# Performance work log

Measured on AMD Instinct MI355X. Metric: run time of the kernel, lower is better.

The kernel has to match this reference:

```python
import jax, jax.numpy as jnp
import numpy as np

N, E, B, BLOCK = 100000, 1600000, 8, 12500
IN, HID, K, OUT = 128, 128, 4, 2
EPS = 1e-15


def setup_inputs() -> dict:
    key = jax.random.key(0)
    ks = jax.random.split(key, 14)
    x = jax.random.normal(ks[0], (N, IN), jnp.float32)
    # edges constrained within each graph's contiguous node block
    src = jax.random.randint(ks[1], (E,), 0, N)
    off = jax.random.randint(ks[2], (E,), 0, BLOCK)
    dst = (src // BLOCK) * BLOCK + off
    edge_index = jnp.stack([src, dst])
    batch = jnp.arange(N) // BLOCK
    s = 0.02
    params = dict(
        W_root1=jax.random.normal(ks[3], (IN, HID), jnp.float32) * s,
        W_rel1=jax.random.normal(ks[4], (IN, HID), jnp.float32) * s,
        b_rel1=jnp.zeros((HID,), jnp.float32),
        W_pool=jax.random.normal(ks[5], (HID, K), jnp.float32) * s,
        b_pool=jnp.zeros((K,), jnp.float32),
        W_rel3=jax.random.normal(ks[6], (HID, HID), jnp.float32) * s,
        b_rel3=jnp.zeros((HID,), jnp.float32),
        W_root3=jax.random.normal(ks[7], (HID, HID), jnp.float32) * s,
        W_lin1=jax.random.normal(ks[8], (HID, HID), jnp.float32) * s,
        b_lin1=jnp.zeros((HID,), jnp.float32),
        W_lin2=jax.random.normal(ks[9], (HID, OUT), jnp.float32) * s,
        b_lin2=jnp.zeros((OUT,), jnp.float32),
    )
    return dict(x=x, edge_index=edge_index, batch=batch, **params)


def _forward(x, edge_index, batch, W_root1, W_rel1, b_rel1, W_pool, b_pool,
             W_rel3, b_rel3, W_root3, W_lin1, b_lin1, W_lin2, b_lin2):
    src, dst = edge_index[0], edge_index[1]
    # GraphConv (aggr='add'): lin_rel(sum_j x_j) + lin_root(x)
    agg = jax.ops.segment_sum(x[src], dst, num_segments=N)  # [N, IN]
    h = jax.nn.relu(agg @ W_rel1 + b_rel1 + x @ W_root1)    # [N, HID]
    # cluster assignment
    s = jax.nn.softmax(h @ W_pool + b_pool, axis=-1)        # [N, K]
    # pooled node features: out[b] = S_b^T X_b  -> [B, K, HID]
    out = jax.ops.segment_sum(s[:, :, None] * h[:, None, :], batch, num_segments=B)
    # coarsened adjacency: out_adj[b] = S_b^T A_b S_b (A[dst, src] = 1 per edge)
    e_graph = batch[dst]
    contrib = s[dst][:, :, None] * s[src][:, None, :]       # [E, K, K]
    out_adj = jax.ops.segment_sum(contrib, e_graph, num_segments=B)  # [B, K, K]
    # mincut loss
    mincut_num = jnp.einsum('bkk->b', out_adj)
    deg = jax.ops.segment_sum(jnp.ones((E,), x.dtype), dst, num_segments=N)
    mincut_den = jax.ops.segment_sum(deg * jnp.sum(s * s, axis=-1), batch, num_segments=B)
    mc_loss = jnp.mean(-(mincut_num / mincut_den))
    # orthogonality loss
    ss = jax.ops.segment_sum(s[:, :, None] * s[:, None, :], batch, num_segments=B)  # [B,K,K]
    ss_norm = jnp.linalg.norm(ss, axis=(1, 2), keepdims=True)
    i_s = jnp.eye(K, dtype=x.dtype)
    o_loss = jnp.mean(jnp.linalg.norm(ss / ss_norm - i_s / jnp.sqrt(jnp.float32(K)), axis=(1, 2)))
    # fix and normalize coarsened adjacency
    out_adj = out_adj * (1.0 - i_s)  # zero diagonal
    d = jnp.sqrt(jnp.sum(out_adj, axis=-1)) + EPS  # [B, K]
    out_adj = out_adj / d[:, None, :] / d[:, :, None]
    # DenseGraphConv (aggr='add'): lin_rel(adj @ x) + lin_root(x)
    x2 = jnp.einsum('bkl,blc->bkc', out_adj, out) @ W_rel3 + b_rel3 + out @ W_root3
    x2 = jnp.mean(x2, axis=1)  # [B, HID]
    x2 = jax.nn.relu(x2 @ W_lin1 + b_lin1)
    logits = x2 @ W_lin2 + b_lin2
    return jax.nn.log_softmax(logits, axis=-1), mc_loss, o_loss, s, out_adj


def reference(x, edge_index, batch, W_root1, W_rel1, b_rel1, W_pool, b_pool,
              W_rel3, b_rel3, W_root3, W_lin1, b_lin1, W_lin2, b_lin2):
    return _forward(x, edge_index, batch, W_root1, W_rel1, b_rel1, W_pool, b_pool,
                    W_rel3, b_rel3, W_root3, W_lin1, b_lin1, W_lin2, b_lin2)
```

## Files before the change

kernel.cpp:

```cpp
#include <hip/hip_runtime.h>

#define NN     100000
#define EE     1600000
#define NB     8
#define BLK    12500
#define HID    128
#define KC     4
#define CHUNKS 196
#define NTILE  49
#define NBIN   392
#define GCAPS  5120

typedef __attribute__((ext_vector_type(8))) short bf16x8;
typedef __attribute__((ext_vector_type(4))) float f32x4;

__device__ __forceinline__ ushort f2bf(float f) {
  uint u = __float_as_uint(f);
  return (ushort)((u + 0x7FFFu + ((u >> 16) & 1u)) >> 16);
}
__device__ __forceinline__ float bf2f(ushort h) {
  return __uint_as_float(((uint)h) << 16);
}

#define GLL16(g, l) \
  __builtin_amdgcn_global_load_lds((const __attribute__((address_space(1))) void*)(g), \
                                   (__attribute__((address_space(3))) void*)(l), 16, 0, 0)

__global__ __launch_bounds__(256) void k_prep_x(const float4* __restrict__ x4,
                                                ushort* __restrict__ xb) {
  int i = blockIdx.x * 256 + threadIdx.x;
  float4 v = x4[i];
  ushort4 r;
  r.x = f2bf(v.x); r.y = f2bf(v.y); r.z = f2bf(v.z); r.w = f2bf(v.w);
  *(ushort4*)(xb + (size_t)i * 4) = r;
}

__global__ __launch_bounds__(256) void k_prep_w(const float* __restrict__ Wrel1,
                                                const float* __restrict__ Wroot1,
                                                ushort* __restrict__ Wt) {
  int col = blockIdx.x, k = threadIdx.x;
  float v = (k < 128) ? Wrel1[k * 128 + col] : Wroot1[(k - 128) * 128 + col];
  Wt[col * 256 + k] = f2bf(v);
}

__global__ __launch_bounds__(256) void k_bucket2(const int* __restrict__ ei,
                                                 int* __restrict__ sbcnt,
                                                 uint* __restrict__ gbuf) {
  __shared__ uint stage[8192];
  __shared__ int cnt[NBIN], start[NBIN + 1], rbase[NBIN];
  __shared__ int gtot[8], gb[8];
  const int t = threadIdx.x;
  for (int b = t; b < NBIN; b += 256) cnt[b] = 0;
  __syncthreads();
  const int e0 = blockIdx.x * 8192;
  uint pk[32]; int br[32];
#pragma unroll
  for (int i = 0; i < 32; ++i) {
    int e = e0 + i * 256 + t;
    bool val = (e < EE);
    int src = 0, dst = 0;
    if (val) {
      src = __builtin_nontemporal_load(ei + e);
      dst = __builtin_nontemporal_load(ei + EE + e);
    }
    int g = dst / BLK;
    int dl = dst - g * BLK;
    int sl = src - g * BLK;
    int bin = g * NTILE + (dl >> 8);
    pk[i] = ((uint)sl << 16) | (uint)dl;
    br[i] = val ? ((bin << 14) | atomicAdd(&cnt[bin], 1)) : -1;
  }
  __syncthreads();
  if (t < 8) {
    int s = 0;
    for (int k = 0; k < NTILE; ++k) s += cnt[t * NTILE + k];
    gtot[t] = s;
  }
  __syncthreads();
  if (t == 0) {
    int s = 0;
    for (int g = 0; g < 8; ++g) { gb[g] = s; s += gtot[g]; }
    start[NBIN] = s;
  }
  __syncthreads();
  if (t < 8) {
    int run = gb[t];
    for (int k = 0; k < NTILE; ++k) { start[t * NTILE + k] = run; run += cnt[t * NTILE + k]; }
  }
  __syncthreads();
  for (int b = t; b < NBIN; b += 256) rbase[b] = atomicAdd(&sbcnt[b], cnt[b]);
#pragma unroll
  for (int i = 0; i < 32; ++i) {
    if (br[i] >= 0) {
      int bin = br[i] >> 14, rank = br[i] & 16383;
      stage[start[bin] + rank] = pk[i];
    }
  }
  __syncthreads();
  const int total = start[NBIN];
  for (int j = t; j < total; j += 256) {
    int lo = 0, hi = NBIN - 1;
    while (lo < hi) { int mid = (lo + hi + 1) >> 1; if (j >= start[mid]) lo = mid; else hi = mid - 1; }
    gbuf[(size_t)lo * GCAPS + rbase[lo] + (j - start[lo])] = stage[j];
  }
}

__global__ __launch_bounds__(512) void k_scan392(const int* __restrict__ sbcnt,
                                                 int* __restrict__ sbbase) {
  __shared__ int sd[512];
  const int t = threadIdx.x;
  int v = (t < NBIN) ? sbcnt[t] : 0;
  sd[t] = v;
  __syncthreads();
  for (int s = 1; s < 512; s <<= 1) {
    int x = (t >= s) ? sd[t - s] : 0;
    __syncthreads();
    sd[t] += x;
    __syncthreads();
  }
  if (t < NBIN) sbbase[t] = sd[t] - v;
}

__global__ __launch_bounds__(256) void k_csr_tile(const uint* __restrict__ gbuf,
                                                  const int* __restrict__ sbcnt,
                                                  const int* __restrict__ sbbase,
                                                  int* __restrict__ rowptr,
                                                  int* __restrict__ count,
                                                  int* __restrict__ csr) {
  const int g = blockIdx.x & 7;
  const int tile = blockIdx.x >> 3;
  const int bin = g * NTILE + tile;
  const int m = sbcnt[bin];
  const int base = sbbase[bin];
  const int n0t = tile * 256;
  const int nt = min(256, BLK - n0t);
  __shared__ uint ent[GCAPS];
  __shared__ ushort srt[GCAPS];
  __shared__ int cnt[256], scn[256], cur[256];
  const int t = threadIdx.x;
  cnt[t] = 0;
  __syncthreads();
  const uint* buf = gbuf + (size_t)bin * GCAPS;
  for (int i = t; i < m; i += 256) {
    uint pk = buf[i];
    ent[i] = pk;
    atomicAdd(&cnt[(int)(pk & 0xFFFFu) - n0t], 1);
  }
  __syncthreads();
  int v = cnt[t];
  scn[t] = v;
  __syncthreads();
  for (int s = 1; s < 256; s <<= 1) {
    int x = (t >= s) ? scn[t - s] : 0;
    __syncthreads();
    scn[t] += x;
    __syncthreads();
  }
  int excl = scn[t] - v;
  cur[t] = excl;
  if (t < nt) {
    rowptr[g * BLK + n0t + t] = base + excl;
    count[g * BLK + n0t + t] = v;
  }
  __syncthreads();
  for (int i = t; i < m; i += 256) {
    uint pk = ent[i];
    int p = atomicAdd(&cur[(int)(pk & 0xFFFFu) - n0t], 1);
    srt[p] = (ushort)(pk >> 16);
  }
  __syncthreads();
  const int nb = g * BLK;
  for (int i = t; i < m; i += 256)
    csr[base + i] = nb + (int)srt[i];
}

__global__ __launch_bounds__(256) void k_agg2(const ushort* __restrict__ xb,
                                              const int* __restrict__ count,
                                              const int* __restrict__ rowptr,
                                              const int* __restrict__ csr,
                                              ushort* __restrict__ aggb) {
  const int xg = blockIdx.x & 7;
  const int j = blockIdx.x >> 3;
  const int half = threadIdx.x >> 5;
  const int lane = threadIdx.x & 31;
  const int ln = j * 8 + half;
  if (ln >= BLK) return;
  const int node = xg * BLK + ln;
  const int deg = count[node];
  const int* sl = csr + rowptr[node];
  int idx0 = (lane < deg) ? sl[lane] : 0;
  int idx1 = (32 + lane < deg) ? sl[32 + lane] : 0;

#define GETIDX(e) ((e) < 32 ? __shfl(idx0, (e), 32) \
                            : ((e) < 64 ? __shfl(idx1, (e) - 32, 32) : sl[(e)]))

  float A0 = 0.f, A1 = 0.f, A2 = 0.f, A3 = 0.f;
  float B0 = 0.f, B1 = 0.f, B2 = 0.f, B3 = 0.f;
  float C0 = 0.f, C1 = 0.f, C2 = 0.f, C3 = 0.f;
  float D0 = 0.f, D1 = 0.f, D2 = 0.f, D3 = 0.f;
  int e = 0;
  for (; e + 4 <= deg; e += 4) {
    int s0 = GETIDX(e + 0);
    int s1 = GETIDX(e + 1);
    int s2 = GETIDX(e + 2);
    int s3 = GETIDX(e + 3);
    ushort4 v0 = *(const ushort4*)(xb + (size_t)s0 * HID + lane * 4);
    ushort4 v1 = *(const ushort4*)(xb + (size_t)s1 * HID + lane * 4);
    ushort4 v2 = *(const ushort4*)(xb + (size_t)s2 * HID + lane * 4);
    ushort4 v3 = *(const ushort4*)(xb + (size_t)s3 * HID + lane * 4);
    A0 += bf2f(v0.x); A1 += bf2f(v0.y); A2 += bf2f(v0.z); A3 += bf2f(v0.w);
    B0 += bf2f(v1.x); B1 += bf2f(v1.y); B2 += bf2f(v1.z); B3 += bf2f(v1.w);
    C0 += bf2f(v2.x); C1 += bf2f(v2.y); C2 += bf2f(v2.z); C3 += bf2f(v2.w);
    D0 += bf2f(v3.x); D1 += bf2f(v3.y); D2 += bf2f(v3.z); D3 += bf2f(v3.w);
  }
  for (; e < deg; ++e) {
    int s0 = GETIDX(e);
    ushort4 v0 = *(const ushort4*)(xb + (size_t)s0 * HID + lane * 4);
    A0 += bf2f(v0.x); A1 += bf2f(v0.y); A2 += bf2f(v0.z); A3 += bf2f(v0.w);
  }
#undef GETIDX

  ushort* dstp = aggb + (size_t)node * HID + lane * 4;
  ushort4 r;
  r.x = f2bf(A0 + B0 + C0 + D0);
  r.y = f2bf(A1 + B1 + C1 + D1);
  r.z = f2bf(A2 + B2 + C2 + D2);
  r.w = f2bf(A3 + B3 + C3 + D3);
  *(ushort4*)dstp = r;
}

__global__ __launch_bounds__(256) void k_fused(
    const ushort* __restrict__ aggb, const ushort* __restrict__ xb,
    const ushort* __restrict__ Wt, const float* __restrict__ brel1,
    const float* __restrict__ Wpool, const float* __restrict__ bpool,
    const int* __restrict__ count, float* __restrict__ s_out,
    float* __restrict__ out_pool, float* __restrict__ ss_g,
    float* __restrict__ den_g) {
  __shared__ ushort Aag_s[64][128];
  __shared__ ushort Ax_s[64][128];
  __shared__ ushort hLb[64][136];
  __shared__ float outL[KC][HID];
  __shared__ float ssL[16];
  __shared__ float denL;

  const int t = threadIdx.x;
  const int bi = blockIdx.x;
  const int bG = bi & 7;
  const int chunk = bi >> 3;
  const int node0 = bG * BLK + chunk * 64;
  int nrows = BLK - chunk * 64;
  if (nrows > 64) nrows = 64;

  const int w = t >> 6;
  const int l = t & 63;

  {
    const int sub = l >> 4;
    const int c16 = l & 15;
#pragma unroll
    for (int i = 0; i < 4; ++i) {
      const int j = w * 4 + i;
      const int row = j * 4 + sub;
      const int rs = (row < nrows) ? row : (nrows - 1);
      const int boff = (c16 * 16) ^ ((row & 7) << 4);
      const ushort* ga = aggb + (size_t)(node0 + rs) * HID + (boff >> 1);
      const ushort* gx = xb + (size_t)(node0 + rs) * HID + (boff >> 1);
      GLL16(ga, &Aag_s[j * 4][0]);
      GLL16(gx, &Ax_s[j * 4][0]);
    }
  }

  for (int i = t; i < KC * HID; i += 256) ((float*)outL)[i] = 0.f;
  if (t < 16) ssL[t] = 0.f;
  if (t == 0) denL = 0.f;

  const int m16 = l & 15;
  const int gq = l >> 4;

  bf16x8 Breg[8][2];
#pragma unroll
  for (int kt = 0; kt < 8; ++kt)
#pragma unroll
    for (int fc = 0; fc < 2; ++fc)
      Breg[kt][fc] =
          *(const bf16x8*)(Wt + (size_t)(32 * w + 16 * fc + m16) * 256 + kt * 32 + 8 * gq);

  f32x4 acc[4][2];
#pragma unroll
  for (int fr = 0; fr < 4; ++fr)
#pragma unroll
    for (int fc = 0; fc < 2; ++fc) acc[fr][fc] = (f32x4){0.f, 0.f, 0.f, 0.f};

  asm volatile("s_waitcnt vmcnt(0)" ::: "memory");
  __syncthreads();

#pragma unroll
  for (int kt = 0; kt < 8; ++kt) {
    const int k4 = kt & 3;
    bf16x8 af[4];
#pragma unroll
    for (int fr = 0; fr < 4; ++fr) {
      const int r = 16 * fr + m16;
      const int ci = (k4 * 32 + gq * 8) ^ ((r & 7) << 3);
      af[fr] = (kt < 4) ? *(const bf16x8*)&Aag_s[r][ci]
                        : *(const bf16x8*)&Ax_s[r][ci];
    }
#pragma unroll
    for (int fr = 0; fr < 4; ++fr)
#pragma unroll
      for (int fc = 0; fc < 2; ++fc)
        acc[fr][fc] = __builtin_amdgcn_mfma_f32_16x16x32_bf16(af[fr], Breg[kt][fc],
                                                              acc[fr][fc], 0, 0, 0);
  }

  const float bc0 = brel1[32 * w + m16];
  const float bc1 = brel1[32 * w + 16 + m16];
#pragma unroll
  for (int fr = 0; fr < 4; ++fr)
#pragma unroll
    for (int fc = 0; fc < 2; ++fc)
#pragma unroll
      for (int r = 0; r < 4; ++r)
        hLb[16 * fr + 4 * gq + r][32 * w + 16 * fc + m16] =
            f2bf(fmaxf(acc[fr][fc][r] + (fc ? bc1 : bc0), 0.f));
  __syncthreads();

  const int g4 = t >> 4;
  const int c0 = (t & 15) << 2;
  const int li = t & 15;

  float h[4][8];
#pragma unroll
  for (int r = 0; r < 4; ++r) {
    ushort4 v0 = *(const ushort4*)&hLb[g4 * 4 + r][c0];
    ushort4 v1 = *(const ushort4*)&hLb[g4 * 4 + r][c0 + 64];
    h[r][0] = bf2f(v0.x); h[r][1] = bf2f(v0.y); h[r][2] = bf2f(v0.z); h[r][3] = bf2f(v0.w);
    h[r][4] = bf2f(v1.x); h[r][5] = bf2f(v1.y); h[r][6] = bf2f(v1.z); h[r][7] = bf2f(v1.w);
  }

  float wp[8][4];
#pragma unroll
  for (int j = 0; j < 8; ++j) {
    int col = c0 + (j & 3) + (j >> 2) * 64;
    float4 v = *(const float4*)(Wpool + col * 4);
    wp[j][0] = v.x; wp[j][1] = v.y; wp[j][2] = v.z; wp[j][3] = v.w;
  }
  float pp[4][4];
#pragma unroll
  for (int r = 0; r < 4; ++r)
#pragma unroll
    for (int k = 0; k < 4; ++k) pp[r][k] = 0.f;
#pragma unroll
  for (int r = 0; r < 4; ++r)
#pragma unroll
    for (int j = 0; j < 8; ++j)
#pragma unroll
      for (int k = 0; k < 4; ++k) pp[r][k] = fmaf(h[r][j], wp[j][k], pp[r][k]);
#pragma unroll
  for (int m = 1; m <= 8; m <<= 1)
#pragma unroll
    for (int r = 0; r < 4; ++r)
#pragma unroll
      for (int k = 0; k < 4; ++k) pp[r][k] += __shfl_xor(pp[r][k], m);

  float4 bp4 = *(const float4*)bpool;
  float bp[4] = {bp4.x, bp4.y, bp4.z, bp4.w};
  float sv[4][4];
#pragma unroll
  for (int r = 0; r < 4; ++r) {
    float p[4];
#pragma unroll
    for (int k = 0; k < 4; ++k) p[k] = pp[r][k] + bp[k];
    float mx = fmaxf(fmaxf(p[0], p[1]), fmaxf(p[2], p[3]));
    float e0 = expf(p[0] - mx), e1 = expf(p[1] - mx), e2 = expf(p[2] - mx), e3 = expf(p[3] - mx);
    float inv = 1.f / (e0 + e1 + e2 + e3);
    float valid = (g4 * 4 + r < nrows) ? 1.f : 0.f;
    sv[r][0] = e0 * inv * valid; sv[r][1] = e1 * inv * valid;
    sv[r][2] = e2 * inv * valid; sv[r][3] = e3 * inv * valid;
  }

  {
    int rW = li >> 2, kW = li & 3;
    if (g4 * 4 + rW < nrows) {
      int node = node0 + g4 * 4 + rW;
      float val = 0.f;
#pragma unroll
      for (int rr = 0; rr < 4; ++rr)
#pragma unroll
        for (int kk = 0; kk < 4; ++kk)
          if (li == rr * 4 + kk) val = sv[rr][kk];
      s_out[node * 4 + kW] = val;
    }
  }

  {
    int k1 = li >> 2, k2 = li & 3;
    float a1[4], a2[4];
#pragma unroll
    for (int rr = 0; rr < 4; ++rr) {
      float v1 = 0.f, v2 = 0.f;
#pragma unroll
      for (int kk = 0; kk < 4; ++kk) {
        if (k1 == kk) v1 = sv[rr][kk];
        if (k2 == kk) v2 = sv[rr][kk];
      }
      a1[rr] = v1; a2[rr] = v2;
    }
    float ssv = a1[0] * a2[0] + a1[1] * a2[1] + a1[2] * a2[2] + a1[3] * a2[3];
    atomicAdd(&ssL[li], ssv);
  }

  if (li == 0) {
    float dent = 0.f;
#pragma unroll
    for (int rr = 0; rr < 4; ++rr) {
      int rowg = g4 * 4 + rr;
      if (rowg < nrows) {
        float dg = (float)count[node0 + rowg];
        dent += dg * (sv[rr][0] * sv[rr][0] + sv[rr][1] * sv[rr][1] +
                      sv[rr][2] * sv[rr][2] + sv[rr][3] * sv[rr][3]);
      }
    }
    atomicAdd(&denL, dent);
  }

  float po[4][8];
#pragma unroll
  for (int k = 0; k < 4; ++k)
#pragma unroll
    for (int c = 0; c < 8; ++c) po[k][c] = 0.f;
#pragma unroll
  for (int k = 0; k < 4; ++k)
#pragma unroll
    for (int rr = 0; rr < 4; ++rr)
#pragma unroll
      for (int c = 0; c < 8; ++c) po[k][c] = fmaf(sv[rr][k], h[rr][c], po[k][c]);
#pragma unroll
  for (int k = 0; k < 4; ++k)
#pragma unroll
    for (int c = 0; c < 8; ++c) {
      po[k][c] += __shfl_xor(po[k][c], 16);
      po[k][c] += __shfl_xor(po[k][c], 32);
    }
  if ((t & 63) < 16) {
#pragma unroll
    for (int k = 0; k < 4; ++k)
#pragma unroll
      for (int c = 0; c < 8; ++c)
        atomicAdd(&outL[k][c0 + (c & 3) + (c >> 2) * 64], po[k][c]);
  }

  __syncthreads();
  for (int i = t; i < KC * HID; i += 256)
    atomicAdd(&out_pool[bG * KC * HID + i], ((const float*)outL)[i]);
  if (t < 16) atomicAdd(&ss_g[bG * 16 + t], ssL[t]);
  if (t == 0) atomicAdd(&den_g[bG], denL);
}

__global__ __launch_bounds__(256) void k_adj2(const int* __restrict__ count,
                                              const int* __restrict__ rowptr,
                                              const int* __restrict__ csr,
                                              const float* __restrict__ s,
                                              float* __restrict__ adjraw) {
  __shared__ float accL[4][2][16];
  const int t = threadIdx.x;
  if (t < 128) ((float*)accL)[t] = 0.f;
  __syncthreads();
  const int node = blockIdx.x * 256 + t;
  const int g0 = (blockIdx.x * 256) / BLK;
  if (node < NN) {
    const int gi = node / BLK - g0;
    const int deg = count[node];
    const int* sl = csr + rowptr[node];
    float A0 = 0.f, A1 = 0.f, A2 = 0.f, A3 = 0.f;
    float B0 = 0.f, B1 = 0.f, B2 = 0.f, B3 = 0.f;
    float C0 = 0.f, C1 = 0.f, C2 = 0.f, C3 = 0.f;
    float D0 = 0.f, D1 = 0.f, D2 = 0.f, D3 = 0.f;
    int e = 0;
    for (; e + 4 <= deg; e += 4) {
      int s0 = sl[e + 0], s1 = sl[e + 1], s2 = sl[e + 2], s3 = sl[e + 3];
      float4 v0 = *(const float4*)(s + (size_t)s0 * 4);
      float4 v1 = *(const float4*)(s + (size_t)s1 * 4);
      float4 v2 = *(const float4*)(s + (size_t)s2 * 4);
      float4 v3 = *(const float4*)(s + (size_t)s3 * 4);
      A0 += v0.x; A1 += v0.y; A2 += v0.z; A3 += v0.w;
      B0 += v1.x; B1 += v1.y; B2 += v1.z; B3 += v1.w;
      C0 += v2.x; C1 += v2.y; C2 += v2.z; C3 += v2.w;
      D0 += v3.x; D1 += v3.y; D2 += v3.z; D3 += v3.w;
    }
    for (; e < deg; ++e) {
      float4 v0 = *(const float4*)(s + (size_t)sl[e] * 4);
      A0 += v0.x; A1 += v0.y; A2 += v0.z; A3 += v0.w;
    }
    float t0 = A0 + B0 + C0 + D0;
    float t1 = A1 + B1 + C1 + D1;
    float t2 = A2 + B2 + C2 + D2;
    float t3 = A3 + B3 + C3 + D3;
    float4 sn = *(const float4*)(s + (size_t)node * 4);
    float* base = accL[t >> 6][gi];
#pragma unroll
    for (int i = 0; i < 16; ++i) {
      int idx = (i + t) & 15;
      int hi = idx >> 2, lo = idx & 3;
      float a = (hi == 0) ? sn.x : (hi == 1) ? sn.y : (hi == 2) ? sn.z : sn.w;
      float b = (lo == 0) ? t0 : (lo == 1) ? t1 : (lo == 2) ? t2 : t3;
      atomicAdd(base + idx, a * b);
    }
  }
  __syncthreads();
  if (t < 32) {
    int gi = t >> 4, i = t & 15, gg = g0 + gi;
    if (gg < NB) {
      float v = accL[0][gi][i] + accL[1][gi][i] + accL[2][gi][i] + accL[3][gi][i];
      atomicAdd(&adjraw[gg * 16 + i], v);
    }
  }
}

__global__ __launch_bounds__(128) void k_graph(
    const float* __restrict__ out_pool, const float* __restrict__ adjraw,
    const float* __restrict__ den_g, const float* __restrict__ ss_g,
    const float* __restrict__ Wrel3, const float* __restrict__ brel3,
    const float* __restrict__ Wroot3, const float* __restrict__ Wlin1,
    const float* __restrict__ blin1, const float* __restrict__ Wlin2,
    const float* __restrict__ blin2, float* __restrict__ d_out,
    float* __restrict__ scratch) {
  const int b = blockIdx.x, t = threadIdx.x;
  __shared__ float adjL[16], adjnL[16], dL[4];
  __shared__ float osL[128], msL[128], x2mL[128], x3L[128];
  if (t < 16) adjL[t] = adjraw[b * 16 + t];
  __syncthreads();
  if (t < 4) {
    float srow = 0.f;
#pragma unroll
    for (int l = 0; l < 4; ++l)
      if (l != t) srow += adjL[t * 4 + l];
    dL[t] = sqrtf(srow) + 1e-15f;
  }
  __syncthreads();
  if (t < 16) {
    int k1 = t >> 2, k2 = t & 3;
    float az = (k1 == k2) ? 0.f : adjL[t];
    float an = az / (dL[k2] * dL[k1]);
    adjnL[t] = an;
    d_out[400018 + b * 16 + t] = an;
  }
  __syncthreads();
  float o0 = out_pool[b * 512 + 0 * 128 + t];
  float o1 = out_pool[b * 512 + 1 * 128 + t];
  float o2 = out_pool[b * 512 + 2 * 128 + t];
  float o3 = out_pool[b * 512 + 3 * 128 + t];
  float m0 = adjnL[0] * o0 + adjnL[1] * o1 + adjnL[2] * o2 + adjnL[3] * o3;
  float m1 = adjnL[4] * o0 + adjnL[5] * o1 + adjnL[6] * o2 + adjnL[7] * o3;
  float m2 = adjnL[8] * o0 + adjnL[9] * o1 + adjnL[10] * o2 + adjnL[11] * o3;
  float m3 = adjnL[12] * o0 + adjnL[13] * o1 + adjnL[14] * o2 + adjnL[15] * o3;
  osL[t] = o0 + o1 + o2 + o3;
  msL[t] = m0 + m1 + m2 + m3;
  __syncthreads();
  float accc = brel3[t];
  for (int j = 0; j < 128; ++j)
    accc += 0.25f * (msL[j] * Wrel3[j * 128 + t] + osL[j] * Wroot3[j * 128 + t]);
  x2mL[t] = accc;
  __syncthreads();
  float a2 = blin1[t];
  for (int j = 0; j < 128; ++j) a2 += x2mL[j] * Wlin1[j * 128 + t];
  x3L[t] = fmaxf(a2, 0.f);
  __syncthreads();
  if (t < 2) {
    float lg = blin2[t];
    for (int j = 0; j < 128; ++j) lg += x3L[j] * Wlin2[j * 2 + t];
    scratch[b * 2 + t] = lg;
  }
  if (t == 0) {
    float tr = adjL[0] + adjL[5] + adjL[10] + adjL[15];
    scratch[16 + b] = tr / den_g[b];
    float n2 = 0.f;
    for (int i = 0; i < 16; ++i) { float v = ss_g[b * 16 + i]; n2 += v * v; }
    float nn = sqrtf(n2);
    float od = 0.f;
    for (int i = 0; i < 16; ++i) {
      float v = ss_g[b * 16 + i] / nn - (((i >> 2) == (i & 3)) ? 0.5f : 0.f);
      od += v * v;
    }
    scratch[24 + b] = sqrtf(od);
  }
}

__global__ void k_final(const float* __restrict__ scratch, float* __restrict__ d_out) {
  if (threadIdx.x == 0 && blockIdx.x == 0) {
    float mc = 0.f, oo = 0.f;
    for (int b = 0; b < NB; ++b) { mc += scratch[16 + b]; oo += scratch[24 + b]; }
    d_out[16] = -(mc / (float)NB);
    d_out[17] = oo / (float)NB;
    for (int b = 0; b < NB; ++b) {
      float l0 = scratch[2 * b], l1 = scratch[2 * b + 1];
      float m = fmaxf(l0, l1);
      float lse = m + logf(expf(l0 - m) + expf(l1 - m));
      d_out[2 * b] = l0 - lse;
      d_out[2 * b + 1] = l1 - lse;
    }
  }
}

extern "C" void kernel_launch(void* const* d_in, const int* in_sizes, int n_in,
                              void* d_out, int out_size, void* d_ws, size_t ws_size,
                              hipStream_t stream) {
  (void)in_sizes; (void)n_in; (void)out_size; (void)ws_size;
  const float* x      = (const float*)d_in[0];
  const int*   ei     = (const int*)d_in[1];
  const float* Wroot1 = (const float*)d_in[3];
  const float* Wrel1  = (const float*)d_in[4];
  const float* brel1  = (const float*)d_in[5];
  const float* Wpool  = (const float*)d_in[6];
  const float* bpool  = (const float*)d_in[7];
  const float* Wrel3  = (const float*)d_in[8];
  const float* brel3  = (const float*)d_in[9];
  const float* Wroot3 = (const float*)d_in[10];
  const float* Wlin1  = (const float*)d_in[11];
  const float* blin1  = (const float*)d_in[12];
  const float* Wlin2  = (const float*)d_in[13];
  const float* blin2  = (const float*)d_in[14];
  float* out = (float*)d_out;

  char* ws = (char*)d_ws;
  float*  out_pool = (float*)(ws + 0);
  float*  ss_g     = (float*)(ws + 16384);
  float*  adjraw   = (float*)(ws + 16896);
  float*  den_g    = (float*)(ws + 17408);
  float*  scratch  = (float*)(ws + 17440);
  int*    sbcnt    = (int*)(ws + 17568);
  int*    sbbase   = (int*)(ws + 19136);
  int*    count    = (int*)(ws + 20736);
  int*    rowptr   = (int*)(ws + 420736);
  ushort* Wt       = (ushort*)(ws + 820752);
  int*    csr      = (int*)(ws + 886288);
  ushort* xb       = (ushort*)(ws + 7286288);
  ushort* aggb     = (ushort*)(ws + 32886288);
  uint*   gbuf     = (uint*)(ws + 58486288);

  hipMemsetAsync(ws, 0, 19136, stream);
  k_prep_x<<<12500, 256, 0, stream>>>((const float4*)x, xb);
  k_prep_w<<<128, 256, 0, stream>>>(Wrel1, Wroot1, Wt);
  k_bucket2<<<196, 256, 0, stream>>>(ei, sbcnt, gbuf);
  k_scan392<<<1, 512, 0, stream>>>(sbcnt, sbbase);
  k_csr_tile<<<NBIN, 256, 0, stream>>>(gbuf, sbcnt, sbbase, rowptr, count, csr);
  k_agg2<<<8 * ((BLK + 7) / 8), 256, 0, stream>>>(xb, count, rowptr, csr, aggb);
  k_fused<<<NB * CHUNKS, 256, 0, stream>>>(aggb, xb, Wt, brel1, Wpool, bpool, count,
                                           out + 18, out_pool, ss_g, den_g);
  k_adj2<<<(NN + 255) / 256, 256, 0, stream>>>(count, rowptr, csr, out + 18, adjraw);
  k_graph<<<NB, 128, 0, stream>>>(out_pool, adjraw, den_g, ss_g, Wrel3, brel3, Wroot3,
                                  Wlin1, blin1, Wlin2, blin2, out, scratch);
  k_final<<<1, 64, 0, stream>>>(scratch, out);
}
```

Measured before the change: 212.7 us.

## Split fused GEMM/epilogue kernel, widen aggregation unroll, simplify bucket scatter

Splits the fused GraphConv GEMM and the pooling/softmax epilogue into two kernels, with h going through a new bf16 global buffer. The neighbour aggregation loop now issues 8 gathers per iteration instead of 4 to raise memory-level parallelism. The bucket scatter drops its per-element binary search and has each thread copy one bin serially. The split adds an extra kernel launch and a round trip of h through global memory. The serial per-bin copy can also be less coalesced and load-imbalanced.

```diff
diff --git a/kernel.cpp b/kernel.cpp
--- a/kernel.cpp
+++ b/kernel.cpp
@@ -97,11 +97,11 @@
     }
   }
   __syncthreads();
-  const int total = start[NBIN];
-  for (int j = t; j < total; j += 256) {
-    int lo = 0, hi = NBIN - 1;
-    while (lo < hi) { int mid = (lo + hi + 1) >> 1; if (j >= start[mid]) lo = mid; else hi = mid - 1; }
-    gbuf[(size_t)lo * GCAPS + rbase[lo] + (j - start[lo])] = stage[j];
+  for (int b = t; b < NBIN; b += 256) {
+    const int n = cnt[b];
+    const int s0 = start[b];
+    uint* dst = gbuf + (size_t)b * GCAPS + rbase[b];
+    for (int i = 0; i < n; ++i) dst[i] = stage[s0 + i];
   }
 }
 
@@ -194,54 +194,50 @@
 #define GETIDX(e) ((e) < 32 ? __shfl(idx0, (e), 32) \
                             : ((e) < 64 ? __shfl(idx1, (e) - 32, 32) : sl[(e)]))
 
-  float A0 = 0.f, A1 = 0.f, A2 = 0.f, A3 = 0.f;
-  float B0 = 0.f, B1 = 0.f, B2 = 0.f, B3 = 0.f;
-  float C0 = 0.f, C1 = 0.f, C2 = 0.f, C3 = 0.f;
-  float D0 = 0.f, D1 = 0.f, D2 = 0.f, D3 = 0.f;
+  float acc[8][4];
+#pragma unroll
+  for (int q = 0; q < 8; ++q)
+#pragma unroll
+    for (int c = 0; c < 4; ++c) acc[q][c] = 0.f;
+
   int e = 0;
-  for (; e + 4 <= deg; e += 4) {
-    int s0 = GETIDX(e + 0);
-    int s1 = GETIDX(e + 1);
-    int s2 = GETIDX(e + 2);
-    int s3 = GETIDX(e + 3);
-    ushort4 v0 = *(const ushort4*)(xb + (size_t)s0 * HID + lane * 4);
-    ushort4 v1 = *(const ushort4*)(xb + (size_t)s1 * HID + lane * 4);
-    ushort4 v2 = *(const ushort4*)(xb + (size_t)s2 * HID + lane * 4);
-    ushort4 v3 = *(const ushort4*)(xb + (size_t)s3 * HID + lane * 4);
-    A0 += bf2f(v0.x); A1 += bf2f(v0.y); A2 += bf2f(v0.z); A3 += bf2f(v0.w);
-    B0 += bf2f(v1.x); B1 += bf2f(v1.y); B2 += bf2f(v1.z); B3 += bf2f(v1.w);
-    C0 += bf2f(v2.x); C1 += bf2f(v2.y); C2 += bf2f(v2.z); C3 += bf2f(v2.w);
-    D0 += bf2f(v3.x); D1 += bf2f(v3.y); D2 += bf2f(v3.z); D3 += bf2f(v3.w);
+  for (; e + 8 <= deg; e += 8) {
+    int si[8];
+#pragma unroll
+    for (int q = 0; q < 8; ++q) si[q] = GETIDX(e + q);
+    ushort4 v[8];
+#pragma unroll
+    for (int q = 0; q < 8; ++q)
+      v[q] = *(const ushort4*)(xb + (size_t)si[q] * HID + lane * 4);
+#pragma unroll
+    for (int q = 0; q < 8; ++q) {
+      acc[q][0] += bf2f(v[q].x); acc[q][1] += bf2f(v[q].y);
+      acc[q][2] += bf2f(v[q].z); acc[q][3] += bf2f(v[q].w);
+    }
   }
   for (; e < deg; ++e) {
     int s0 = GETIDX(e);
     ushort4 v0 = *(const ushort4*)(xb + (size_t)s0 * HID + lane * 4);
-    A0 += bf2f(v0.x); A1 += bf2f(v0.y); A2 += bf2f(v0.z); A3 += bf2f(v0.w);
+    acc[0][0] += bf2f(v0.x); acc[0][1] += bf2f(v0.y);
+    acc[0][2] += bf2f(v0.z); acc[0][3] += bf2f(v0.w);
   }
 #undef GETIDX
 
-  ushort* dstp = aggb + (size_t)node * HID + lane * 4;
+  float r0 = 0.f, r1 = 0.f, r2 = 0.f, r3 = 0.f;
+#pragma unroll
+  for (int q = 0; q < 8; ++q) { r0 += acc[q][0]; r1 += acc[q][1]; r2 += acc[q][2]; r3 += acc[q][3]; }
   ushort4 r;
-  r.x = f2bf(A0 + B0 + C0 + D0);
-  r.y = f2bf(A1 + B1 + C1 + D1);
-  r.z = f2bf(A2 + B2 + C2 + D2);
-  r.w = f2bf(A3 + B3 + C3 + D3);
-  *(ushort4*)dstp = r;
-}
-
-__global__ __launch_bounds__(256) void k_fused(
+  r.x = f2bf(r0); r.y = f2bf(r1); r.z = f2bf(r2); r.w = f2bf(r3);
+  *(ushort4*)(aggb + (size_t)node * HID + lane * 4) = r;
+}
+
+__global__ __launch_bounds__(256) void k_gemm(
     const ushort* __restrict__ aggb, const ushort* __restrict__ xb,
     const ushort* __restrict__ Wt, const float* __restrict__ brel1,
-    const float* __restrict__ Wpool, const float* __restrict__ bpool,
-    const int* __restrict__ count, float* __restrict__ s_out,
-    float* __restrict__ out_pool, float* __restrict__ ss_g,
-    float* __restrict__ den_g) {
+    ushort* __restrict__ hbuf) {
   __shared__ ushort Aag_s[64][128];
   __shared__ ushort Ax_s[64][128];
   __shared__ ushort hLb[64][136];
-  __shared__ float outL[KC][HID];
-  __shared__ float ssL[16];
-  __shared__ float denL;
 
   const int t = threadIdx.x;
   const int bi = blockIdx.x;
@@ -270,10 +266,6 @@
     }
   }
 
-  for (int i = t; i < KC * HID; i += 256) ((float*)outL)[i] = 0.f;
-  if (t < 16) ssL[t] = 0.f;
-  if (t == 0) denL = 0.f;
-
   const int m16 = l & 15;
   const int gq = l >> 4;
 
@@ -323,6 +315,53 @@
       for (int r = 0; r < 4; ++r)
         hLb[16 * fr + 4 * gq + r][32 * w + 16 * fc + m16] =
             f2bf(fmaxf(acc[fr][fc][r] + (fc ? bc1 : bc0), 0.f));
+  __syncthreads();
+
+  {
+    const int row = t >> 2;
+    const int ch = (t & 3) * 32;
+    if (row < nrows) {
+      ushort* dst = hbuf + (size_t)(node0 + row) * HID + ch;
+      const ushort* src = &hLb[row][ch];
+#pragma unroll
+      for (int q = 0; q < 4; ++q)
+        *(bf16x8*)(dst + q * 8) = *(const bf16x8*)(src + q * 8);
+    }
+  }
+}
+
+__global__ __launch_bounds__(256) void k_epi(
+    const ushort* __restrict__ hbuf, const float* __restrict__ Wpool,
+    const float* __restrict__ bpool, const int* __restrict__ count,
+    float* __restrict__ s_out, float* __restrict__ out_pool,
+    float* __restrict__ ss_g, float* __restrict__ den_g) {
+  __shared__ ushort hLb[64][136];
+  __shared__ float outL[KC][HID];
+  __shared__ float ssL[16];
+  __shared__ float denL;
+
+  const int t = threadIdx.x;
+  const int bi = blockIdx.x;
+  const int bG = bi & 7;
+  const int chunk = bi >> 3;
+  const int node0 = bG * BLK + chunk * 64;
+  int nrows = BLK - chunk * 64;
+  if (nrows > 64) nrows = 64;
+
+  {
+    const int row = t >> 2;
+    const int ch = (t & 3) * 32;
+    const int rs = (row < nrows) ? row : (nrows - 1);
+    const ushort* src = hbuf + (size_t)(node0 + rs) * HID + ch;
+    ushort* dst = &hLb[row][ch];
+#pragma unroll
+    for (int q = 0; q < 4; ++q)
+      *(bf16x8*)(dst + q * 8) = *(const bf16x8*)(src + q * 8);
+  }
+
+  for (int i = t; i < KC * HID; i += 256) ((float*)outL)[i] = 0.f;
+  if (t < 16) ssL[t] = 0.f;
+  if (t == 0) denL = 0.f;
   __syncthreads();
 
   const int g4 = t >> 4;
@@ -637,6 +676,7 @@
   ushort* xb       = (ushort*)(ws + 7286288);
   ushort* aggb     = (ushort*)(ws + 32886288);
   uint*   gbuf     = (uint*)(ws + 58486288);
+  ushort* hbuf     = (ushort*)(ws + 66514448);
 
   hipMemsetAsync(ws, 0, 19136, stream);
   k_prep_x<<<12500, 256, 0, stream>>>((const float4*)x, xb);
@@ -645,8 +685,9 @@
   k_scan392<<<1, 512, 0, stream>>>(sbcnt, sbbase);
   k_csr_tile<<<NBIN, 256, 0, stream>>>(gbuf, sbcnt, sbbase, rowptr, count, csr);
   k_agg2<<<8 * ((BLK + 7) / 8), 256, 0, stream>>>(xb, count, rowptr, csr, aggb);
-  k_fused<<<NB * CHUNKS, 256, 0, stream>>>(aggb, xb, Wt, brel1, Wpool, bpool, count,
-                                           out + 18, out_pool, ss_g, den_g);
+  k_gemm<<<NB * CHUNKS, 256, 0, stream>>>(aggb, xb, Wt, brel1, hbuf);
+  k_epi<<<NB * CHUNKS, 256, 0, stream>>>(hbuf, Wpool, bpool, count, out + 18,
+                                         out_pool, ss_g, den_g);
   k_adj2<<<(NN + 255) / 256, 256, 0, stream>>>(count, rowptr, csr, out + 18, adjraw);
   k_graph<<<NB, 128, 0, stream>>>(out_pool, adjraw, den_g, ss_g, Wrel3, brel3, Wroot3,
                                   Wlin1, blin1, Wlin2, blin2, out, scratch);
```

New measurement: 209.8 us. Within noise of the previous version (-1.4%).
